# Kernel tuning notes

Hardware: AMD Instinct MI355X
Metric: run time of the kernel (lower is better)

The kernel has to match this reference:

```python
import jax, jax.numpy as jnp
import numpy as np

D = 768
H = 12
HD = D // H
FF = 3072
EPS = 1e-5


def layernorm(x, g, b):
    mu = jnp.mean(x, axis=-1, keepdims=True)
    var = jnp.mean(jnp.square(x - mu), axis=-1, keepdims=True)
    return (x - mu) * jax.lax.rsqrt(var + EPS) * g + b


def setup_inputs() -> dict:
    key = jax.random.key(0)
    ks = jax.random.split(key, 12)
    s = 0.02
    return {
        "x": jax.random.normal(ks[0], (4, 1024, D), dtype=jnp.float32),
        "w_qkv": jax.random.normal(ks[1], (D, 3 * D), dtype=jnp.float32) * s,
        "b_qkv": jnp.zeros((3 * D,), jnp.float32),
        "w_proj": jax.random.normal(ks[2], (D, D), dtype=jnp.float32) * s,
        "b_proj": jnp.zeros((D,), jnp.float32),
        "w1": jax.random.normal(ks[3], (D, FF), dtype=jnp.float32) * s,
        "b1": jnp.zeros((FF,), jnp.float32),
        "w2": jax.random.normal(ks[4], (FF, D), dtype=jnp.float32) * s,
        "b2": jnp.zeros((D,), jnp.float32),
        "g1": jnp.ones((D,), jnp.float32),
        "be1": jnp.zeros((D,), jnp.float32),
        "g2": jnp.ones((D,), jnp.float32),
        "be2": jnp.zeros((D,), jnp.float32),
    }


def reference(x, w_qkv, b_qkv, w_proj, b_proj, w1, b1, w2, b2, g1, be1, g2, be2):
    B, N, C = x.shape
    # --- attention (pre-norm) ---
    h = layernorm(x, g1, be1)
    qkv = (h @ w_qkv + b_qkv).reshape(B, N, 3, H, HD)
    q = jnp.transpose(qkv[:, :, 0], (0, 2, 1, 3))  # [B,H,N,hd]
    k = jnp.transpose(qkv[:, :, 1], (0, 2, 1, 3))
    v = jnp.transpose(qkv[:, :, 2], (0, 2, 1, 3))
    attn = jnp.einsum("bhqd,bhkd->bhqk", q, k) * (HD ** -0.5)
    attn = jax.nn.softmax(attn, axis=-1)
    o = jnp.einsum("bhqk,bhkd->bhqd", attn, v)
    o = jnp.transpose(o, (0, 2, 1, 3)).reshape(B, N, C)
    x = x + (o @ w_proj + b_proj)
    # --- feedforward (pre-norm) ---
    h2 = layernorm(x, g2, be2)
    ff = jax.nn.gelu(h2 @ w1 + b1, approximate=False) @ w2 + b2
    return x + ff
```

## Files before the change

kernel.cpp:

```cpp
#include <hip/hip_runtime.h>
#include <hip/hip_bf16.h>
#include <math.h>

typedef __attribute__((ext_vector_type(8))) short short8;
typedef __attribute__((ext_vector_type(4))) float f32x4;

#define DMODEL 768
#define THREE_D 2304
#define FFDIM 3072
#define NSEQ 1024
#define NHEAD 12
#define HEADD 64
#define MROWS 4096

__device__ __forceinline__ ushort f2bf(float f) {
  union { float f; unsigned u; } c; c.f = f;
  unsigned u = c.u;
  unsigned r = (u + 0x7fffu + ((u >> 16) & 1u)) >> 16;
  return (ushort)r;
}

__device__ __forceinline__ unsigned pack2bf(float a, float b) {
  union { __hip_bfloat162 h; unsigned u; } c;
  c.h = __float22bfloat162_rn(make_float2(a, b));
  return c.u;
}

__device__ __forceinline__ void load_lds16(const ushort* g, const ushort* l) {
  __builtin_amdgcn_global_load_lds(
      (const __attribute__((address_space(1))) unsigned int*)g,
      (__attribute__((address_space(3))) unsigned int*)l, 16, 0, 0);
}

template <int N> __device__ __forceinline__ void wait_vm() {
  if constexpr (N == 8)      asm volatile("s_waitcnt vmcnt(8)" ::: "memory");
  else if constexpr (N == 6) asm volatile("s_waitcnt vmcnt(6)" ::: "memory");
  else if constexpr (N == 4) asm volatile("s_waitcnt vmcnt(4)" ::: "memory");
  else                       asm volatile("s_waitcnt vmcnt(0)" ::: "memory");
}

__device__ __forceinline__ void ln_body(const float* __restrict__ x,
    const float* __restrict__ g, const float* __restrict__ be,
    ushort* __restrict__ out, int row, int tid,
    float* red1, float* red2) {
  const float* xr = x + (size_t)row * DMODEL;
  float v0 = xr[tid], v1 = xr[tid + 256], v2 = xr[tid + 512];
  float s = v0 + v1 + v2;
  #pragma unroll
  for (int off = 32; off; off >>= 1) s += __shfl_xor(s, off);
  if ((tid & 63) == 0) red1[tid >> 6] = s;
  __syncthreads();
  float mean = (red1[0] + red1[1] + red1[2] + red1[3]) * (1.0f / 768.0f);
  float d0 = v0 - mean, d1 = v1 - mean, d2 = v2 - mean;
  float q = d0 * d0 + d1 * d1 + d2 * d2;
  #pragma unroll
  for (int off = 32; off; off >>= 1) q += __shfl_xor(q, off);
  if ((tid & 63) == 0) red2[tid >> 6] = q;
  __syncthreads();
  float var = (red2[0] + red2[1] + red2[2] + red2[3]) * (1.0f / 768.0f);
  float rs = rsqrtf(var + 1e-5f);
  size_t base = (size_t)row * DMODEL;
  out[base + tid]       = f2bf(d0 * rs * g[tid]       + be[tid]);
  out[base + tid + 256] = f2bf(d1 * rs * g[tid + 256] + be[tid + 256]);
  out[base + tid + 512] = f2bf(d2 * rs * g[tid + 512] + be[tid + 512]);
}

__global__ __launch_bounds__(256) void ln_kernel(const float* __restrict__ x,
    const float* __restrict__ g, const float* __restrict__ be,
    ushort* __restrict__ out) {
  __shared__ float red1[4], red2[4];
  ln_body(x, g, be, out, blockIdx.x, threadIdx.x, red1, red2);
}

__global__ __launch_bounds__(256) void pre_kernel(
    const float* __restrict__ w_qkv, const float* __restrict__ w_proj,
    const float* __restrict__ w1, const float* __restrict__ w2,
    ushort* __restrict__ Wqkv_t, ushort* __restrict__ Wproj_t,
    ushort* __restrict__ W1_t, ushort* __restrict__ W2_t,
    const float* __restrict__ x, const float* __restrict__ g1,
    const float* __restrict__ be1, ushort* __restrict__ hbuf) {
  __shared__ float t[32][33];
  int id = blockIdx.x;
  int tid = threadIdx.x;
  if (id >= 6912) {
    ln_body(x, g1, be1, hbuf, id - 6912, tid, &t[0][0], &t[1][0]);
    return;
  }
  const float* W; ushort* Wt; int K, N, bx, by;
  if (id < 1728)      { W = w_qkv;  Wt = Wqkv_t;  K = 768;  N = 2304; bx = id % 72; by = id / 72; }
  else if (id < 2304) { id -= 1728; W = w_proj; Wt = Wproj_t; K = 768;  N = 768;  bx = id % 24; by = id / 24; }
  else if (id < 4608) { id -= 2304; W = w1;     Wt = W1_t;    K = 768;  N = 3072; bx = id % 96; by = id / 96; }
  else                { id -= 4608; W = w2;     Wt = W2_t;    K = 3072; N = 768;  bx = id % 24; by = id / 24; }
  int n0 = bx * 32, k0 = by * 32;
  int tx = tid & 31, ty = tid >> 5;
  #pragma unroll
  for (int r = 0; r < 4; r++)
    t[ty + r * 8][tx] = W[(size_t)(k0 + ty + r * 8) * N + n0 + tx];
  __syncthreads();
  #pragma unroll
  for (int r = 0; r < 4; r++)
    Wt[(size_t)(n0 + ty + r * 8) * K + k0 + tx] = f2bf(t[tx][ty + r * 8]);
}

__global__ void vt_kernel(const ushort* __restrict__ qkv, ushort* __restrict__ Vt) {
  __shared__ ushort t[32][33];
  int n0 = blockIdx.x * 32, d0 = blockIdx.y * 32, bh = blockIdx.z;
  int b = bh / NHEAD, hh = bh % NHEAD;
  int tx = threadIdx.x, ty = threadIdx.y;
  #pragma unroll
  for (int r = 0; r < 4; r++)
    t[ty + r * 8][tx] = qkv[(size_t)(b * NSEQ + n0 + ty + r * 8) * THREE_D +
                            2 * DMODEL + hh * HEADD + d0 + tx];
  __syncthreads();
  #pragma unroll
  for (int r = 0; r < 4; r++) {
    int n = n0 + tx;
    int np = (n & ~63) | (((n & 15) << 2) | ((n >> 4) & 3));
    Vt[((size_t)bh * HEADD + d0 + ty + r * 8) * NSEQ + np] = t[tx][ty + r * 8];
  }
}

template <int BN, int MODE>
__global__ __launch_bounds__(512, 2) void gemm256_kernel(
    const ushort* __restrict__ A, const ushort* __restrict__ Bt,
    const float* __restrict__ bias, void* __restrict__ Cout,
    int gx, int Ntot, int K) {
  constexpr int FN = BN / 64;
  constexpr int WN = BN / 4;
  constexpr int ABUF = (256 + BN) * 64;
  constexpr int BOFF = 256 * 64;
  __shared__ ushort S[2 * ABUF];
  int tid = threadIdx.x, lane = tid & 63, wave = tid >> 6;
  int wm = wave >> 2, wn = wave & 3;
  int rsel = lane & 15, quad = lane >> 4;
  int nwg = gridDim.x;
  int o = blockIdx.x;
  int wg = (o & 7) * (nwg >> 3) + (o >> 3);
  int bx = wg % gx, by = wg / gx;
  int m0 = by * 256, n0 = bx * BN;
  f32x4 acc[8][FN] = {};
  int xorc = (rsel & 7) * 8;

  auto SA = [&](int buf, int k0, int i) {
    int c0 = i * 512 + wave * 64;
    int c = c0 + lane, r = c >> 3;
    int kk = ((c ^ r) & 7) * 8;
    load_lds16(&A[(size_t)(m0 + r) * K + k0 + kk], S + buf * ABUF + c0 * 8);
  };
  auto SB = [&](int buf, int k0, int i) {
    int c0 = i * 512 + wave * 64;
    int c = c0 + lane, r = c >> 3;
    int kk = ((c ^ r) & 7) * 8;
    load_lds16(&Bt[(size_t)(n0 + r) * K + k0 + kk],
               S + buf * ABUF + BOFF + c0 * 8);
  };
  auto RDA = [&](int cur, int half, int ks, int mi) -> short8 {
    int R = wm * 128 + (half * 4 + mi) * 16 + rsel;
    return *(const short8*)&S[cur * ABUF + R * 64 + ((ks * 32 + quad * 8) ^ xorc)];
  };
  auto RDB = [&](int cur, int ks, int ni) -> short8 {
    int R = wn * WN + ni * 16 + rsel;
    return *(const short8*)&S[cur * ABUF + BOFF + R * 64 +
                              ((ks * 32 + quad * 8) ^ xorc)];
  };

  #pragma unroll
  for (int i = 0; i < 4; i++) SA(0, 0, i);
  #pragma unroll
  for (int i = 0; i < FN; i++) SB(0, 0, i);
  wait_vm<0>();
  __builtin_amdgcn_s_barrier();

  int ntk = K >> 6;
  for (int t = 0; t < ntk; t++) {
    int cur = t & 1, nxt = cur ^ 1;
    bool pre = (t + 1 < ntk);
    int nk0 = (t + 1) * 64;
    short8 afb[2][4], bfb[2][FN];
    #pragma unroll
    for (int mi = 0; mi < 4; mi++) afb[0][mi] = RDA(cur, 0, 0, mi);
    #pragma unroll
    for (int ni = 0; ni < FN; ni++) bfb[0][ni] = RDB(cur, 0, ni);
    #pragma unroll
    for (int p = 0; p < 4; p++) {
      const int ks = p >> 1, half = p & 1;
      if (p < 3) {
        const int ksn = (p + 1) >> 1, halfn = (p + 1) & 1;
        #pragma unroll
        for (int mi = 0; mi < 4; mi++)
          afb[(p + 1) & 1][mi] = RDA(cur, halfn, ksn, mi);
        if (p == 1) {
          #pragma unroll
          for (int ni = 0; ni < FN; ni++) bfb[1][ni] = RDB(cur, 1, ni);
        }
      }
      if (pre) {
        if (p == 0) {
          #pragma unroll
          for (int i = 0; i < FN; i++) SB(nxt, nk0, i);
          SA(nxt, nk0, 0);
        } else if (p == 1) {
          SA(nxt, nk0, 1); SA(nxt, nk0, 2); SA(nxt, nk0, 3);
        }
      }
      __builtin_amdgcn_s_setprio(1);
      #pragma unroll
      for (int mi = 0; mi < 4; mi++)
        #pragma unroll
        for (int ni = 0; ni < FN; ni++)
          acc[half * 4 + mi][ni] = __builtin_amdgcn_mfma_f32_16x16x32_bf16(
              afb[p & 1][mi], bfb[ks][ni], acc[half * 4 + mi][ni], 0, 0, 0);
      __builtin_amdgcn_s_setprio(0);
    }
    wait_vm<0>();
    __builtin_amdgcn_s_barrier();
  }
  ushort* Cl = S;
  float bv[FN];
  #pragma unroll
  for (int ni = 0; ni < FN; ni++) bv[ni] = bias[n0 + wn * WN + ni * 16 + rsel];
  #pragma unroll
  for (int mi = 0; mi < 8; mi++) {
    int row = wm * 128 + mi * 16 + quad * 4;
    #pragma unroll
    for (int ni = 0; ni < FN; ni++) {
      int col = wn * WN + ni * 16 + rsel;
      #pragma unroll
      for (int j = 0; j < 4; j++) {
        float v = acc[mi][ni][j] + bv[ni];
        if (MODE == 2) v = 0.5f * v * (1.0f + erff(v * 0.70710678118654752f));
        Cl[(row + j) * 200 + col] = f2bf(v);
      }
    }
  }
  __syncthreads();
  constexpr int CPR = BN / 8;
  ushort* Cg = (ushort*)Cout;
  for (int c = tid; c < 256 * CPR; c += 512) {
    int row = c / CPR, off = c - row * CPR;
    int4 v = *(const int4*)&Cl[row * 200 + off * 8];
    *(int4*)&Cg[(size_t)(m0 + row) * Ntot + n0 + off * 8] = v;
  }
}

template <int BM, int BN>
__global__ __launch_bounds__(256) void gemm_kernel(
    const ushort* __restrict__ A, const ushort* __restrict__ Bt,
    const float* __restrict__ bias, const float* __restrict__ resid,
    float* __restrict__ Cout, int gx, int Ntot, int K) {
  constexpr int ABUF = (BM + BN) * 64;
  constexpr int BOFF = BM * 64;
  constexpr int CSTR = BN + 4;
  constexpr int SMEM = (2 * ABUF * 2 > BM * CSTR * 4) ? 2 * ABUF
                                                      : BM * CSTR * 2;
  __shared__ ushort S[SMEM];
  constexpr int WM = BM / 2, WN = BN / 2;
  constexpr int FM = WM / 16, FN = WN / 16;
  constexpr int NL = BM / 32 + BN / 32;
  int tid = threadIdx.x, lane = tid & 63, wave = tid >> 6;
  int wm = wave >> 1, wn = wave & 1;
  int rsel = lane & 15, quad = lane >> 4;
  int nwg = gridDim.x;
  int o = blockIdx.x;
  int wg = (o & 7) * (nwg >> 3) + (o >> 3);
  int bx = wg % gx, by = wg / gx;
  int m0 = by * BM, n0 = bx * BN;
  f32x4 acc[FM][FN] = {};

  auto STAGE = [&](int buf, int k0) {
    #pragma unroll
    for (int i = 0; i < BM / 32; i++) {
      int c0 = i * 256 + wave * 64;
      int c = c0 + lane, r = c >> 3;
      int kk = ((c ^ r) & 7) * 8;
      load_lds16(&A[(size_t)(m0 + r) * K + k0 + kk], S + buf * ABUF + c0 * 8);
    }
    #pragma unroll
    for (int i = 0; i < BN / 32; i++) {
      int c0 = i * 256 + wave * 64;
      int c = c0 + lane, r = c >> 3;
      int kk = ((c ^ r) & 7) * 8;
      load_lds16(&Bt[(size_t)(n0 + r) * K + k0 + kk],
                 S + buf * ABUF + BOFF + c0 * 8);
    }
  };

  STAGE(0, 0);
  int ntk = K >> 6;
  for (int t = 0; t < ntk; t++) {
    int cur = t & 1;
    if (t + 1 < ntk) {
      STAGE(cur ^ 1, (t + 1) * 64);
      wait_vm<NL>();
    } else {
      wait_vm<0>();
    }
    __builtin_amdgcn_s_barrier();
    short8 af[2][FM], bf[2][FN];
    #pragma unroll
    for (int ks = 0; ks < 2; ks++) {
      int ko = ks * 32 + quad * 8;
      #pragma unroll
      for (int mi = 0; mi < FM; mi++) {
        int R = wm * WM + mi * 16 + rsel;
        af[ks][mi] = *(const short8*)&S[cur * ABUF + R * 64 + (ko ^ ((R & 7) * 8))];
      }
      #pragma unroll
      for (int ni = 0; ni < FN; ni++) {
        int R = wn * WN + ni * 16 + rsel;
        bf[ks][ni] = *(const short8*)&S[cur * ABUF + BOFF + R * 64 + (ko ^ ((R & 7) * 8))];
      }
    }
    #pragma unroll
    for (int ks = 0; ks < 2; ks++)
      #pragma unroll
      for (int mi = 0; mi < FM; mi++)
        #pragma unroll
        for (int ni = 0; ni < FN; ni++)
          acc[mi][ni] = __builtin_amdgcn_mfma_f32_16x16x32_bf16(
              af[ks][mi], bf[ks][ni], acc[mi][ni], 0, 0, 0);
    asm volatile("s_waitcnt lgkmcnt(0)" ::: "memory");
    __builtin_amdgcn_s_barrier();
  }
  float* Cl = (float*)S;
  #pragma unroll
  for (int ni = 0; ni < FN; ni++) {
    int col = wn * WN + ni * 16 + rsel;
    float bvv = bias[n0 + col];
    #pragma unroll
    for (int mi = 0; mi < FM; mi++) {
      int row = wm * WM + mi * 16 + quad * 4;
      #pragma unroll
      for (int j = 0; j < 4; j++)
        Cl[(row + j) * CSTR + col] = acc[mi][ni][j] + bvv;
    }
  }
  __syncthreads();
  constexpr int CPR = BN / 4;
  for (int c = tid; c < BM * CPR; c += 256) {
    int row = c / CPR, off = c - row * CPR;
    size_t gi = (size_t)(m0 + row) * Ntot + n0 + off * 4;
    float4 v = *(const float4*)&Cl[row * CSTR + off * 4];
    float4 rr = *(const float4*)&resid[gi];
    v.x += rr.x; v.y += rr.y; v.z += rr.z; v.w += rr.w;
    *(float4*)&Cout[gi] = v;
  }
}

__global__ __launch_bounds__(512) void attn_kernel(
    const ushort* __restrict__ qkv, const ushort* __restrict__ Vt,
    ushort* __restrict__ o) {
  __shared__ ushort Klds[2][64][64];
  __shared__ ushort Vlds[2][64][64];
  __shared__ ushort Plds[8][16][72];
  const float CL2 = 0.18033688011112042f;
  int tid = threadIdx.x, lane = tid & 63, wave = tid >> 6;
  int id = blockIdx.x;
  int qt = id / 48, bh = id % 48;
  int b = bh / NHEAD, hh = bh % NHEAD;
  int q0 = qt * 128;
  int rsel = lane & 15, quad = lane >> 4;
  int xorc = (rsel & 7) * 8;

  short8 qf[2];
  {
    int qrow = q0 + wave * 16 + rsel;
    const ushort* qp = qkv + (size_t)(b * NSEQ + qrow) * THREE_D + hh * HEADD + quad * 8;
    qf[0] = *(const short8*)qp;
    qf[1] = *(const short8*)(qp + 32);
  }
  short8 onesf;
  #pragma unroll
  for (int i = 0; i < 8; i++) onesf[i] = (short)0x3F80;

  int r0 = tid >> 3, d0 = (tid & 7) * 8;
  int sw0 = d0 ^ ((r0 & 7) * 8);
  const ushort* Kg = qkv + (size_t)b * NSEQ * THREE_D + DMODEL + hh * HEADD;
  const ushort* Vg = Vt + (size_t)bh * HEADD * NSEQ;
  int4 kr0, vr0;
  auto LD = [&](int kv0) {
    kr0 = *(const int4*)&Kg[(size_t)(kv0 + r0) * THREE_D + d0];
    vr0 = *(const int4*)&Vg[(size_t)r0 * NSEQ + kv0 + d0];
  };
  auto ST = [&](int bf) {
    *(int4*)&Klds[bf][r0][sw0] = kr0;
    *(int4*)&Vlds[bf][r0][sw0] = vr0;
  };

  f32x4 oacc[4] = {};
  f32x4 osum = {};

  LD(0); ST(0); __syncthreads();

  for (int t = 0; t < 16; t++) {
    int bf = t & 1;
    if (t < 15) LD((t + 1) * 64);
    f32x4 sfr[4] = {};
    __builtin_amdgcn_s_setprio(1);
    #pragma unroll
    for (int ks = 0; ks < 2; ks++) {
      int ko = ks * 32 + quad * 8;
      #pragma unroll
      for (int nt = 0; nt < 4; nt++) {
        short8 kf = *(const short8*)&Klds[bf][nt * 16 + rsel][ko ^ xorc];
        sfr[nt] = __builtin_amdgcn_mfma_f32_16x16x32_bf16(qf[ks], kf, sfr[nt], 0, 0, 0);
      }
    }
    __builtin_amdgcn_s_setprio(0);
    #pragma unroll
    for (int i = 0; i < 4; i++) {
      float p0 = exp2f(fmaf(sfr[0][i], CL2, -12.0f));
      float p1 = exp2f(fmaf(sfr[1][i], CL2, -12.0f));
      float p2 = exp2f(fmaf(sfr[2][i], CL2, -12.0f));
      float p3 = exp2f(fmaf(sfr[3][i], CL2, -12.0f));
      uint2 pw = make_uint2(pack2bf(p0, p1), pack2bf(p2, p3));
      *(uint2*)&Plds[wave][quad * 4 + i][rsel * 4] = pw;
    }
    __builtin_amdgcn_s_setprio(1);
    #pragma unroll
    for (int ks = 0; ks < 2; ks++) {
      int ko = ks * 32 + quad * 8;
      short8 pf = *(const short8*)&Plds[wave][rsel][ko];
      #pragma unroll
      for (int nt = 0; nt < 4; nt++) {
        short8 vf = *(const short8*)&Vlds[bf][nt * 16 + rsel][ko ^ xorc];
        oacc[nt] = __builtin_amdgcn_mfma_f32_16x16x32_bf16(pf, vf, oacc[nt], 0, 0, 0);
      }
      osum = __builtin_amdgcn_mfma_f32_16x16x32_bf16(pf, onesf, osum, 0, 0, 0);
    }
    __builtin_amdgcn_s_setprio(0);
    if (t < 15) ST(bf ^ 1);
    __syncthreads();
  }
  float rin[4];
  #pragma unroll
  for (int i = 0; i < 4; i++) rin[i] = __builtin_amdgcn_rcpf(osum[i]);
  #pragma unroll
  for (int nt = 0; nt < 4; nt++)
    #pragma unroll
    for (int i = 0; i < 4; i++) {
      int qrow = q0 + wave * 16 + quad * 4 + i;
      int col = hh * HEADD + nt * 16 + rsel;
      o[(size_t)(b * NSEQ + qrow) * DMODEL + col] = f2bf(oacc[nt][i] * rin[i]);
    }
}

extern "C" void kernel_launch(void* const* d_in, const int* in_sizes, int n_in,
                              void* d_out, int out_size, void* d_ws, size_t ws_size,
                              hipStream_t stream) {
  const float* x      = (const float*)d_in[0];
  const float* w_qkv  = (const float*)d_in[1];
  const float* b_qkv  = (const float*)d_in[2];
  const float* w_proj = (const float*)d_in[3];
  const float* b_proj = (const float*)d_in[4];
  const float* w1     = (const float*)d_in[5];
  const float* b1     = (const float*)d_in[6];
  const float* w2     = (const float*)d_in[7];
  const float* b2     = (const float*)d_in[8];
  const float* g1     = (const float*)d_in[9];
  const float* be1    = (const float*)d_in[10];
  const float* g2     = (const float*)d_in[11];
  const float* be2    = (const float*)d_in[12];
  float* out = (float*)d_out;

  char* ws = (char*)d_ws;
  ushort* Wqkv_t  = (ushort*)(ws + 0);
  ushort* Wproj_t = (ushort*)(ws + 3538944);
  ushort* W1_t    = (ushort*)(ws + 4718592);
  ushort* W2_t    = (ushort*)(ws + 9437184);
  ushort* hbuf    = (ushort*)(ws + 14155776);
  ushort* qkv     = (ushort*)(ws + 20447232);
  ushort* ff1     = qkv;
  ushort* VtB     = (ushort*)(ws + 45613056);
  ushort* obuf    = (ushort*)(ws + 51904512);
  float*  x2      = (float*)(ws + 58195968);

  dim3 tb(32, 8);
  pre_kernel<<<6912 + 4096, 256, 0, stream>>>(
      w_qkv, w_proj, w1, w2, Wqkv_t, Wproj_t, W1_t, W2_t,
      x, g1, be1, hbuf);

  gemm256_kernel<192, 0><<<192, 512, 0, stream>>>(
      hbuf, Wqkv_t, b_qkv, qkv, THREE_D / 192, THREE_D, DMODEL);

  vt_kernel<<<dim3(NSEQ / 32, HEADD / 32, 4 * NHEAD), tb, 0, stream>>>(qkv, VtB);

  attn_kernel<<<384, 512, 0, stream>>>(qkv, VtB, obuf);

  gemm_kernel<128, 64><<<384, 256, 0, stream>>>(
      obuf, Wproj_t, b_proj, x, x2, DMODEL / 64, DMODEL, DMODEL);

  ln_kernel<<<MROWS, 256, 0, stream>>>(x2, g2, be2, hbuf);

  gemm256_kernel<192, 2><<<256, 512, 0, stream>>>(
      hbuf, W1_t, b1, ff1, FFDIM / 192, FFDIM, DMODEL);

  gemm_kernel<128, 64><<<384, 256, 0, stream>>>(
      ff1, W2_t, b2, x2, out, DMODEL / 64, DMODEL, FFDIM);

  (void)in_sizes; (void)n_in; (void)out_size; (void)ws_size;
}
```

Before: 151.8 us.

## Store intermediate residual in bf16 and widen weight transpose tiles

The intermediate residual x2 produced by the projection GEMM is now stored in bf16 instead of fp32. A new bf16 layernorm kernel reads it, and the final GEMM reads it as its bf16 residual, which roughly halves the traffic for that tensor. The weight transpose in pre_kernel now uses 64x32 tiles with float4 loads and 16-byte packed stores, so it launches half as many blocks. Rounding the residual to bf16 adds precision loss to the output.

```diff
diff --git a/kernel.cpp b/kernel.cpp
--- a/kernel.cpp
+++ b/kernel.cpp
@@ -20,6 +20,10 @@
   return (ushort)r;
 }
 
+__device__ __forceinline__ float bf2f(ushort u) {
+  union { float f; unsigned u; } c; c.u = ((unsigned)u) << 16; return c.f;
+}
+
 __device__ __forceinline__ unsigned pack2bf(float a, float b) {
   union { __hip_bfloat162 h; unsigned u; } c;
   c.h = __float22bfloat162_rn(make_float2(a, b));
@@ -65,11 +69,40 @@
   out[base + tid + 512] = f2bf(d2 * rs * g[tid + 512] + be[tid + 512]);
 }
 
-__global__ __launch_bounds__(256) void ln_kernel(const float* __restrict__ x,
-    const float* __restrict__ g, const float* __restrict__ be,
-    ushort* __restrict__ out) {
+__global__ __launch_bounds__(256) void ln_bf16_kernel(
+    const ushort* __restrict__ x, const float* __restrict__ g,
+    const float* __restrict__ be, ushort* __restrict__ out) {
   __shared__ float red1[4], red2[4];
-  ln_body(x, g, be, out, blockIdx.x, threadIdx.x, red1, red2);
+  int row = blockIdx.x, tid = threadIdx.x;
+  const ushort* xr = x + (size_t)row * DMODEL;
+  float v0 = 0.f, v1 = 0.f, v2 = 0.f, v3 = 0.f;
+  if (tid < 192) {
+    ushort4 u = *(const ushort4*)&xr[tid * 4];
+    v0 = bf2f(u.x); v1 = bf2f(u.y); v2 = bf2f(u.z); v3 = bf2f(u.w);
+  }
+  float s = v0 + v1 + v2 + v3;
+  #pragma unroll
+  for (int off = 32; off; off >>= 1) s += __shfl_xor(s, off);
+  if ((tid & 63) == 0) red1[tid >> 6] = s;
+  __syncthreads();
+  float mean = (red1[0] + red1[1] + red1[2] + red1[3]) * (1.0f / 768.0f);
+  float d0 = v0 - mean, d1 = v1 - mean, d2 = v2 - mean, d3 = v3 - mean;
+  float q = (tid < 192) ? d0 * d0 + d1 * d1 + d2 * d2 + d3 * d3 : 0.f;
+  #pragma unroll
+  for (int off = 32; off; off >>= 1) q += __shfl_xor(q, off);
+  if ((tid & 63) == 0) red2[tid >> 6] = q;
+  __syncthreads();
+  float var = (red2[0] + red2[1] + red2[2] + red2[3]) * (1.0f / 768.0f);
+  float rs = rsqrtf(var + 1e-5f);
+  if (tid < 192) {
+    int c = tid * 4;
+    float o0 = d0 * rs * g[c] + be[c];
+    float o1 = d1 * rs * g[c + 1] + be[c + 1];
+    float o2 = d2 * rs * g[c + 2] + be[c + 2];
+    float o3 = d3 * rs * g[c + 3] + be[c + 3];
+    uint2 pw = make_uint2(pack2bf(o0, o1), pack2bf(o2, o3));
+    *(uint2*)&out[(size_t)row * DMODEL + c] = pw;
+  }
 }
 
 __global__ __launch_bounds__(256) void pre_kernel(
@@ -79,27 +112,34 @@
     ushort* __restrict__ W1_t, ushort* __restrict__ W2_t,
     const float* __restrict__ x, const float* __restrict__ g1,
     const float* __restrict__ be1, ushort* __restrict__ hbuf) {
-  __shared__ float t[32][33];
+  __shared__ float t[64][33];
   int id = blockIdx.x;
   int tid = threadIdx.x;
-  if (id >= 6912) {
-    ln_body(x, g1, be1, hbuf, id - 6912, tid, &t[0][0], &t[1][0]);
+  if (id >= 3456) {
+    ln_body(x, g1, be1, hbuf, id - 3456, tid, &t[0][0], &t[1][0]);
     return;
   }
   const float* W; ushort* Wt; int K, N, bx, by;
-  if (id < 1728)      { W = w_qkv;  Wt = Wqkv_t;  K = 768;  N = 2304; bx = id % 72; by = id / 72; }
-  else if (id < 2304) { id -= 1728; W = w_proj; Wt = Wproj_t; K = 768;  N = 768;  bx = id % 24; by = id / 24; }
-  else if (id < 4608) { id -= 2304; W = w1;     Wt = W1_t;    K = 768;  N = 3072; bx = id % 96; by = id / 96; }
-  else                { id -= 4608; W = w2;     Wt = W2_t;    K = 3072; N = 768;  bx = id % 24; by = id / 24; }
-  int n0 = bx * 32, k0 = by * 32;
-  int tx = tid & 31, ty = tid >> 5;
-  #pragma unroll
-  for (int r = 0; r < 4; r++)
-    t[ty + r * 8][tx] = W[(size_t)(k0 + ty + r * 8) * N + n0 + tx];
-  __syncthreads();
-  #pragma unroll
-  for (int r = 0; r < 4; r++)
-    Wt[(size_t)(n0 + ty + r * 8) * K + k0 + tx] = f2bf(t[tx][ty + r * 8]);
+  if (id < 864)       { W = w_qkv;  Wt = Wqkv_t;  K = 768;  N = 2304; bx = id % 72; by = id / 72; }
+  else if (id < 1152) { id -= 864;  W = w_proj; Wt = Wproj_t; K = 768;  N = 768;  bx = id % 24; by = id / 24; }
+  else if (id < 2304) { id -= 1152; W = w1;     Wt = W1_t;    K = 768;  N = 3072; bx = id % 96; by = id / 96; }
+  else                { id -= 2304; W = w2;     Wt = W2_t;    K = 3072; N = 768;  bx = id % 24; by = id / 24; }
+  int n0 = bx * 32, k0 = by * 64;
+  #pragma unroll
+  for (int i = 0; i < 2; i++) {
+    int s = tid + i * 256;
+    int k = s >> 3, nq = (s & 7) * 4;
+    float4 w = *(const float4*)&W[(size_t)(k0 + k) * N + n0 + nq];
+    t[k][nq] = w.x; t[k][nq + 1] = w.y; t[k][nq + 2] = w.z; t[k][nq + 3] = w.w;
+  }
+  __syncthreads();
+  {
+    int n = tid >> 3, kq = (tid & 7) * 8;
+    ushort u[8];
+    #pragma unroll
+    for (int j = 0; j < 8; j++) u[j] = f2bf(t[kq + j][n]);
+    *(int4*)&Wt[(size_t)(n0 + n) * K + k0 + kq] = *(int4*)u;
+  }
 }
 
 __global__ void vt_kernel(const ushort* __restrict__ qkv, ushort* __restrict__ Vt) {
@@ -243,11 +283,11 @@
   }
 }
 
-template <int BM, int BN>
+template <int BM, int BN, int MODE>
 __global__ __launch_bounds__(256) void gemm_kernel(
     const ushort* __restrict__ A, const ushort* __restrict__ Bt,
-    const float* __restrict__ bias, const float* __restrict__ resid,
-    float* __restrict__ Cout, int gx, int Ntot, int K) {
+    const float* __restrict__ bias, const void* __restrict__ resid,
+    void* __restrict__ Cout, int gx, int Ntot, int K) {
   constexpr int ABUF = (BM + BN) * 64;
   constexpr int BOFF = BM * 64;
   constexpr int CSTR = BN + 4;
@@ -341,9 +381,17 @@
     int row = c / CPR, off = c - row * CPR;
     size_t gi = (size_t)(m0 + row) * Ntot + n0 + off * 4;
     float4 v = *(const float4*)&Cl[row * CSTR + off * 4];
-    float4 rr = *(const float4*)&resid[gi];
-    v.x += rr.x; v.y += rr.y; v.z += rr.z; v.w += rr.w;
-    *(float4*)&Cout[gi] = v;
+    if (MODE == 0) {
+      float4 rr = *(const float4*)&((const float*)resid)[gi];
+      v.x += rr.x; v.y += rr.y; v.z += rr.z; v.w += rr.w;
+      uint2 pw = make_uint2(pack2bf(v.x, v.y), pack2bf(v.z, v.w));
+      *(uint2*)&((ushort*)Cout)[gi] = pw;
+    } else {
+      ushort4 rr = *(const ushort4*)&((const ushort*)resid)[gi];
+      v.x += bf2f(rr.x); v.y += bf2f(rr.y);
+      v.z += bf2f(rr.z); v.w += bf2f(rr.w);
+      *(float4*)&((float*)Cout)[gi] = v;
+    }
   }
 }
 
@@ -473,10 +521,10 @@
   ushort* ff1     = qkv;
   ushort* VtB     = (ushort*)(ws + 45613056);
   ushort* obuf    = (ushort*)(ws + 51904512);
-  float*  x2      = (float*)(ws + 58195968);
+  ushort* x2      = (ushort*)(ws + 58195968);
 
   dim3 tb(32, 8);
-  pre_kernel<<<6912 + 4096, 256, 0, stream>>>(
+  pre_kernel<<<3456 + 4096, 256, 0, stream>>>(
       w_qkv, w_proj, w1, w2, Wqkv_t, Wproj_t, W1_t, W2_t,
       x, g1, be1, hbuf);
 
@@ -487,15 +535,15 @@
 
   attn_kernel<<<384, 512, 0, stream>>>(qkv, VtB, obuf);
 
-  gemm_kernel<128, 64><<<384, 256, 0, stream>>>(
+  gemm_kernel<128, 64, 0><<<384, 256, 0, stream>>>(
       obuf, Wproj_t, b_proj, x, x2, DMODEL / 64, DMODEL, DMODEL);
 
-  ln_kernel<<<MROWS, 256, 0, stream>>>(x2, g2, be2, hbuf);
+  ln_bf16_kernel<<<MROWS, 256, 0, stream>>>(x2, g2, be2, hbuf);
 
   gemm256_kernel<192, 2><<<256, 512, 0, stream>>>(
       hbuf, W1_t, b1, ff1, FFDIM / 192, FFDIM, DMODEL);
 
-  gemm_kernel<128, 64><<<384, 256, 0, stream>>>(
+  gemm_kernel<128, 64, 1><<<384, 256, 0, stream>>>(
       ff1, W2_t, b2, x2, out, DMODEL / 64, DMODEL, FFDIM);
 
   (void)in_sizes; (void)n_in; (void)out_size; (void)ws_size;
```

Result: no change. 150.7 us (-0.7%).
